# Kernel optimization log

Hardware: AMD Instinct MI355X
Metric: run time of the kernel (lower is better)

## Reference

```python
import jax, jax.numpy as jnp
import numpy as np

# Grid / module constants (init_kwargs)
SCALE_MULT = 3.0
H, W, D = 200, 200, 16
PC_MIN = np.array([-40.0, -40.0, -1.0], dtype=np.float32)
GRID = 0.4
RADII_MIN = 1
EPS = 1e-8

P, G, C = 16384, 2048, 17


def _quat_to_rot(q):
    # q: (..., 4) normalized quaternion -> (..., 3, 3)
    w, x, y, z = q[..., 0], q[..., 1], q[..., 2], q[..., 3]
    R = jnp.stack([
        1 - 2 * (y * y + z * z), 2 * (x * y - w * z), 2 * (x * z + w * y),
        2 * (x * y + w * z), 1 - 2 * (x * x + z * z), 2 * (y * z - w * x),
        2 * (x * z - w * y), 2 * (y * z + w * x), 1 - 2 * (x * x + y * y),
    ], axis=-1)
    return R.reshape(q.shape[:-1] + (3, 3))


def setup_inputs() -> dict:
    key = jax.random.key(0)
    ks = jax.random.split(key, 8)
    extent = jnp.asarray([H * GRID, W * GRID, D * GRID], jnp.float32)
    pc_min = jnp.asarray(PC_MIN)
    # points and primitive means strictly inside the grid (bounds asserts in the module)
    pts = pc_min + jax.random.uniform(ks[0], (1, P, 3), jnp.float32) * (extent - 1e-3)
    means3D = pc_min + jax.random.uniform(ks[1], (1, G, 3), jnp.float32) * (extent - 1e-3)
    opas = jax.random.uniform(ks[2], (1, G), jnp.float32, 0.05, 0.95)
    u = jax.random.uniform(ks[3], (1, G), jnp.float32, 0.5, 2.0)   # superquadric exponent e1
    v = jax.random.uniform(ks[4], (1, G), jnp.float32, 0.5, 2.0)   # superquadric exponent e2
    semantics = jax.random.normal(ks[5], (1, G, C), jnp.float32)
    scales = jax.random.uniform(ks[6], (1, G, 3), jnp.float32, 0.1, 0.6)
    q = jax.random.normal(ks[7], (1, G, 4), jnp.float32)
    q = q / jnp.linalg.norm(q, axis=-1, keepdims=True)
    rot3D = _quat_to_rot(q)  # (1, G, 3, 3)
    return {"pts": pts, "means3D": means3D, "opas": opas, "u": u, "v": v,
            "semantics": semantics, "scales": scales, "rot3D": rot3D}


def _forward(pts, means3D, opas, u, v, semantics, scales, rot3D):
    # squeeze batch dim of 1 (module asserts pts.shape[0] == 1)
    pts = pts[0]; means3D = means3D[0]; opas = opas[0]
    u = u[0]; v = v[0]; semantics = semantics[0]
    scales = scales[0]; rot3D = rot3D[0]
    pc_min = jnp.asarray(PC_MIN)

    points_int = jnp.floor((pts - pc_min) / GRID).astype(jnp.int32)              # (P,3)
    means_int = jnp.floor((jax.lax.stop_gradient(means3D) - pc_min) / GRID).astype(jnp.int32)  # (G,3)
    radii = jnp.ceil(jax.lax.stop_gradient(scales).max(-1) * SCALE_MULT / GRID).astype(jnp.int32)
    radii = jnp.maximum(radii, RADII_MIN)                                        # (G,)

    # radius-limited neighborhood (Chebyshev distance in voxel space)
    cheb = jnp.abs(points_int[:, None, :] - means_int[None, :, :]).max(-1)       # (P,G)
    mask = cheb <= radii[None, :]

    # local coords: R^T (p - mu), computed without materializing (P,G,3) deltas twice
    local = jnp.einsum('pj,gji->pgi', pts, rot3D) - jnp.einsum('gj,gji->gi', means3D, rot3D)[None]
    s2 = (local / scales[None]) ** 2 + EPS                                       # (P,G,3)

    inv_e1 = (1.0 / u)[None]  # (1,G)
    inv_e2 = (1.0 / v)[None]
    # superquadric inside-outside function
    f = (s2[..., 0] ** inv_e2 + s2[..., 1] ** inv_e2) ** (v / u)[None] + s2[..., 2] ** inv_e1
    a = opas[None] * jnp.exp(-0.5 * f)
    a = jnp.where(mask, a, 0.0)                                                  # (P,G)

    density = a.sum(-1)                                                          # (P,)
    logits = jnp.einsum('pg,gc->pc', a, semantics) / (density[:, None] + 1e-9)   # (P,C)
    a_c = jnp.clip(a, 0.0, 1.0 - 1e-4)
    bin_logits = 1.0 - jnp.exp(jnp.log1p(-a_c).sum(-1))                          # (P,)
    return logits, bin_logits, density


def reference(pts, means3D, opas, u, v, semantics, scales, rot3D):
    return _forward(pts, means3D, opas, u, v, semantics, scales, rot3D)
```

## Files before the change

### kernel.cpp

```cpp
#include <hip/hip_runtime.h>
#include <math.h>

#define NP 16384
#define NG 2048
#define NC 17

#define TSH 3
#define NTX 25
#define NTY 25
#define NTILE (NTX * NTY)
#define SEGC 32
#define CCAP 128
#define ROWF 40

#define GRIDSZ 0.4f
#define PCMINX -40.0f
#define PCMINY -40.0f
#define PCMINZ -1.0f
#define SCALE_MULTC 3.0f


__global__ __launch_bounds__(256)
void bin_kernel(const float* __restrict__ means3D, const float* __restrict__ opas,
                const float* __restrict__ uu, const float* __restrict__ vv,
                const float* __restrict__ semantics, const float* __restrict__ scales,
                const float* __restrict__ rot3D,
                unsigned int* __restrict__ candCnt, float* __restrict__ rowTbl) {
    __shared__ unsigned short candSeg[4][SEGC];
    __shared__ int wc[4];
    const int tid = threadIdx.x;
    const int lane = tid & 63;
    const int w = tid >> 6;
    const int b = blockIdx.x;
    const int tx = b % NTX, ty = b / NTX;

    unsigned cl = 0;
#pragma unroll
    for (int it = 0; it < 8; ++it) {
        int g = w * 512 + it * 64 + lane;
        float mx = means3D[g * 3 + 0], my = means3D[g * 3 + 1];
        float sx = scales[g * 3 + 0], sy = scales[g * 3 + 1], sz = scales[g * 3 + 2];
        int vx = (int)floorf((mx - PCMINX) / GRIDSZ);
        int vy = (int)floorf((my - PCMINY) / GRIDSZ);
        float smax = fmaxf(sx, fmaxf(sy, sz));
        int rad = (int)ceilf(smax * SCALE_MULTC / GRIDSZ);
        if (rad < 1) rad = 1;
        bool ov = (((vx - rad) >> TSH) <= tx) & (((vx + rad) >> TSH) >= tx) &
                  (((vy - rad) >> TSH) <= ty) & (((vy + rad) >> TSH) >= ty);
        unsigned long long bal = __ballot(ov);
        if (ov) {
            int pos = (int)cl + (int)__popcll(bal & ((1ull << lane) - 1ull));
            if (pos < SEGC) candSeg[w][pos] = (unsigned short)g;
        }
        cl += (unsigned)__popcll(bal);
    }
    if (lane == 0) wc[w] = min((int)cl, SEGC);
    __syncthreads();

    const int c0 = wc[0], c1 = wc[1], c2 = wc[2], c3 = wc[3];
    const int o1 = c0, o2 = o1 + c1, o3 = o2 + c2;
    const int total = o3 + c3;

    if (tid < total) {
        int s, idx;
        if (tid < o1)      { s = 0; idx = tid; }
        else if (tid < o2) { s = 1; idx = tid - o1; }
        else if (tid < o3) { s = 2; idx = tid - o2; }
        else               { s = 3; idx = tid - o3; }
        int g = (int)candSeg[s][idx];
        float mx = means3D[g * 3 + 0], my = means3D[g * 3 + 1], mz = means3D[g * 3 + 2];
        float sx = scales[g * 3 + 0], sy = scales[g * 3 + 1], sz = scales[g * 3 + 2];
        float r[9];
#pragma unroll
        for (int i = 0; i < 9; ++i) r[i] = rot3D[g * 9 + i];
        float sem[NC];
#pragma unroll
        for (int c = 0; c < NC; ++c) sem[c] = semantics[(size_t)g * NC + c];
        float ug = uu[g], vg = vv[g], op = opas[g];
        int vx = (int)floorf((mx - PCMINX) / GRIDSZ);
        int vy = (int)floorf((my - PCMINY) / GRIDSZ);
        int vz = (int)floorf((mz - PCMINZ) / GRIDSZ);
        float smax = fmaxf(sx, fmaxf(sy, sz));
        int rad = (int)ceilf(smax * SCALE_MULTC / GRIDSZ);
        if (rad < 1) rad = 1;

        float4* Rv = (float4*)(rowTbl + ((size_t)b * CCAP + tid) * ROWF);
        Rv[0] = make_float4(mx * r[0] + my * r[3] + mz * r[6],
                            mx * r[1] + my * r[4] + mz * r[7],
                            mx * r[2] + my * r[5] + mz * r[8], r[0]);
        Rv[1] = make_float4(r[1], r[2], r[3], r[4]);
        Rv[2] = make_float4(r[5], r[6], r[7], r[8]);
        Rv[3] = make_float4(1.0f / sx, 1.0f / sy, 1.0f / sz, op);
        Rv[4] = make_float4(1.0f / ug, 1.0f / vg, vg / ug, sem[16]);
        Rv[5] = make_float4(sem[0], sem[1], sem[2], sem[3]);
        Rv[6] = make_float4(sem[4], sem[5], sem[6], sem[7]);
        Rv[7] = make_float4(sem[8], sem[9], sem[10], sem[11]);
        Rv[8] = make_float4(sem[12], sem[13], sem[14], sem[15]);
        Rv[9] = make_float4(__int_as_float(vx), __int_as_float(vy),
                            __int_as_float(vz), __int_as_float(rad));
    }
    if (tid == 0) candCnt[b] = (unsigned)total;
}

__device__ __forceinline__ float eval_row(const float* __restrict__ R,
                                          float px, float py, float pz,
                                          int ix, int iy, int iz) {
    const float4* Rv = (const float4*)R;
    float4 f0 = Rv[0], f1 = Rv[1], f2 = Rv[2], f3 = Rv[3], f4 = Rv[4], f9 = Rv[9];
    int cheb = max(max(abs(ix - __float_as_int(f9.x)),
                       abs(iy - __float_as_int(f9.y))),
                   abs(iz - __float_as_int(f9.z)));
    float l0 = px * f0.w + py * f1.z + pz * f2.y - f0.x;
    float l1 = px * f1.x + py * f1.w + pz * f2.z - f0.y;
    float l2 = px * f1.y + py * f2.x + pz * f2.w - f0.z;
    float t0 = l0 * f3.x, t1 = l1 * f3.y, t2 = l2 * f3.z;
    float s0 = t0 * t0 + 1e-8f;
    float s1 = t1 * t1 + 1e-8f;
    float s2 = t2 * t2 + 1e-8f;
    float f = __powf(__powf(s0, f4.y) + __powf(s1, f4.y), f4.z) + __powf(s2, f4.x);
    float a = f3.w * __expf(-0.5f * f);
    return (cheb <= __float_as_int(f9.w)) ? a : 0.0f;
}

__global__ __launch_bounds__(256)
void point_kernel(const float* __restrict__ pts,
                  const unsigned int* __restrict__ candCnt,
                  const float* __restrict__ rowTbl,
                  float* __restrict__ out) {
    const int tid = threadIdx.x;
    const int lane = tid & 63;
    const int w = tid >> 6;
    const int sub = lane >> 4;
    const int k = lane & 15;
    const int p = blockIdx.x * 16 + w * 4 + sub;

    float px = pts[p * 3 + 0], py = pts[p * 3 + 1], pz = pts[p * 3 + 2];
    int ix = (int)floorf((px - PCMINX) / GRIDSZ);
    int iy = (int)floorf((py - PCMINY) / GRIDSZ);
    int iz = (int)floorf((pz - PCMINZ) / GRIDSZ);
    int t = (iy >> TSH) * NTX + (ix >> TSH);
    int n = (int)candCnt[t];
    const float* base = rowTbl + (size_t)t * CCAP * ROWF;

    float dens = 0.0f, lb = 0.0f, acc = 0.0f, acc16 = 0.0f;

    for (int j = 0; j * 16 < n; ++j) {
        int kk = j * 16 + k;
        float a = 0.0f;
        if (kk < n)
            a = eval_row(base + (size_t)kk * ROWF, px, py, pz, ix, iy, iz);
        dens += a;
        lb += __logf(1.0f - fminf(a, 1.0f - 1e-4f));

        int kmax = min(16, n - j * 16);
        for (int kq = 0; kq < kmax; ++kq) {
            float aq = __shfl(a, (sub << 4) + kq);
            const float* R = base + (size_t)(j * 16 + kq) * ROWF;
            acc = fmaf(aq, R[20 + k], acc);
            if (k == 0) acc16 = fmaf(aq, R[19], acc16);
        }
    }

#pragma unroll
    for (int o = 1; o < 16; o <<= 1) {
        dens += __shfl_xor(dens, o);
        lb += __shfl_xor(lb, o);
    }

    float inv = 1.0f / (dens + 1e-9f);
    out[(size_t)p * NC + k] = acc * inv;
    if (k == 0) {
        out[(size_t)p * NC + 16] = acc16 * inv;
        out[(size_t)NP * NC + p] = 1.0f - expf(lb);
        out[(size_t)NP * NC + NP + p] = dens;
    }
}

__global__ __launch_bounds__(64)
void agg_kernel_fb(const float* __restrict__ pts,
                   const float* __restrict__ means3D,
                   const float* __restrict__ opas,
                   const float* __restrict__ uu,
                   const float* __restrict__ vv,
                   const float* __restrict__ semantics,
                   const float* __restrict__ scales,
                   const float* __restrict__ rot3D,
                   float* __restrict__ out) {
    int p = blockIdx.x * 64 + threadIdx.x;
    if (p >= NP) return;
    float px = pts[p * 3 + 0], py = pts[p * 3 + 1], pz = pts[p * 3 + 2];
    int pix = (int)floorf((px - PCMINX) / GRIDSZ);
    int piy = (int)floorf((py - PCMINY) / GRIDSZ);
    int piz = (int)floorf((pz - PCMINZ) / GRIDSZ);
    float density = 0.0f, logbin = 0.0f;
    float acc[NC];
#pragma unroll
    for (int c = 0; c < NC; ++c) acc[c] = 0.0f;
    for (int g = 0; g < NG; ++g) {
        float mx = means3D[g * 3 + 0], my = means3D[g * 3 + 1], mz = means3D[g * 3 + 2];
        float sx = scales[g * 3 + 0], sy = scales[g * 3 + 1], sz = scales[g * 3 + 2];
        int vx = (int)floorf((mx - PCMINX) / GRIDSZ);
        int vy = (int)floorf((my - PCMINY) / GRIDSZ);
        int vz = (int)floorf((mz - PCMINZ) / GRIDSZ);
        float smax = fmaxf(sx, fmaxf(sy, sz));
        int rad = (int)ceilf(smax * SCALE_MULTC / GRIDSZ);
        rad = rad < 1 ? 1 : rad;
        int cheb = max(abs(pix - vx), max(abs(piy - vy), abs(piz - vz)));
        if (cheb <= rad) {
            const float* r = rot3D + (size_t)g * 9;
            float dx = px - mx, dy = py - my, dz = pz - mz;
            float l0 = dx * r[0] + dy * r[3] + dz * r[6];
            float l1 = dx * r[1] + dy * r[4] + dz * r[7];
            float l2 = dx * r[2] + dy * r[5] + dz * r[8];
            float t0 = l0 / sx, t1 = l1 / sy, t2 = l2 / sz;
            float s0 = t0 * t0 + 1e-8f, s1 = t1 * t1 + 1e-8f, s2 = t2 * t2 + 1e-8f;
            float ie1 = 1.0f / uu[g], ie2 = 1.0f / vv[g], e21 = vv[g] * ie1;
            float f = __powf(__powf(s0, ie2) + __powf(s1, ie2), e21) + __powf(s2, ie1);
            float a = opas[g] * __expf(-0.5f * f);
            density += a;
            const float* sg = semantics + (size_t)g * NC;
#pragma unroll
            for (int c = 0; c < NC; ++c) acc[c] = fmaf(a, sg[c], acc[c]);
            logbin += __logf(1.0f - fminf(a, 1.0f - 1e-4f));
        }
    }
    float inv = 1.0f / (density + 1e-9f);
#pragma unroll
    for (int c = 0; c < NC; ++c) out[(size_t)p * NC + c] = acc[c] * inv;
    out[(size_t)NP * NC + p] = 1.0f - expf(logbin);
    out[(size_t)NP * NC + NP + p] = density;
}

extern "C" void kernel_launch(void* const* d_in, const int* in_sizes, int n_in,
                              void* d_out, int out_size, void* d_ws, size_t ws_size,
                              hipStream_t stream) {
    const float* pts       = (const float*)d_in[0];
    const float* means3D   = (const float*)d_in[1];
    const float* opas      = (const float*)d_in[2];
    const float* uu        = (const float*)d_in[3];
    const float* vv        = (const float*)d_in[4];
    const float* semantics = (const float*)d_in[5];
    const float* scales    = (const float*)d_in[6];
    const float* rot3D     = (const float*)d_in[7];
    float* out = (float*)d_out;

    size_t cntBytes = ((size_t)NTILE * sizeof(unsigned int) + 255) & ~(size_t)255;
    size_t rowBytes = (size_t)NTILE * CCAP * ROWF * sizeof(float);
    size_t need = cntBytes + rowBytes;

    if (ws_size >= need) {
        unsigned int* candCnt = (unsigned int*)d_ws;
        float* rowTbl = (float*)((char*)d_ws + cntBytes);
        bin_kernel<<<NTILE, 256, 0, stream>>>(means3D, opas, uu, vv, semantics,
                                              scales, rot3D, candCnt, rowTbl);
        point_kernel<<<NP / 16, 256, 0, stream>>>(pts, candCnt, rowTbl, out);
    } else {
        agg_kernel_fb<<<NP / 64, 64, 0, stream>>>(pts, means3D, opas, uu, vv, semantics,
                                                  scales, rot3D, out);
    }
}
```

Baseline: 29.33 us.

## Pad candidate rows to multiples of 16, unroll accumulation, replace log-sum with product

The bin kernel zero-fills padding rows so each tile's candidate count is a multiple of 16. This lets the aggregation loop drop its bounds checks and fully unroll the 16-step shuffle/accumulate inner loop. The log1p/exp transmittance is replaced by a running product of (1-a) combined with multiplicative shuffles, which removes a log per element and the final exp. The ballot loop is also split from the overlap computation so the global loads can be batched. Zero rows give a=0 through opacity zero, but the product form may underflow differently than the log sum.

```diff
diff --git a/kernel.cpp b/kernel.cpp
--- a/kernel.cpp
+++ b/kernel.cpp
@@ -34,7 +34,7 @@
     const int b = blockIdx.x;
     const int tx = b % NTX, ty = b / NTX;
 
-    unsigned cl = 0;
+    bool ov[8];
 #pragma unroll
     for (int it = 0; it < 8; ++it) {
         int g = w * 512 + it * 64 + lane;
@@ -45,12 +45,16 @@
         float smax = fmaxf(sx, fmaxf(sy, sz));
         int rad = (int)ceilf(smax * SCALE_MULTC / GRIDSZ);
         if (rad < 1) rad = 1;
-        bool ov = (((vx - rad) >> TSH) <= tx) & (((vx + rad) >> TSH) >= tx) &
-                  (((vy - rad) >> TSH) <= ty) & (((vy + rad) >> TSH) >= ty);
-        unsigned long long bal = __ballot(ov);
-        if (ov) {
+        ov[it] = (((vx - rad) >> TSH) <= tx) & (((vx + rad) >> TSH) >= tx) &
+                 (((vy - rad) >> TSH) <= ty) & (((vy + rad) >> TSH) >= ty);
+    }
+    unsigned cl = 0;
+#pragma unroll
+    for (int it = 0; it < 8; ++it) {
+        unsigned long long bal = __ballot(ov[it]);
+        if (ov[it]) {
             int pos = (int)cl + (int)__popcll(bal & ((1ull << lane) - 1ull));
-            if (pos < SEGC) candSeg[w][pos] = (unsigned short)g;
+            if (pos < SEGC) candSeg[w][pos] = (unsigned short)(w * 512 + it * 64 + lane);
         }
         cl += (unsigned)__popcll(bal);
     }
@@ -60,6 +64,7 @@
     const int c0 = wc[0], c1 = wc[1], c2 = wc[2], c3 = wc[3];
     const int o1 = c0, o2 = o1 + c1, o3 = o2 + c2;
     const int total = o3 + c3;
+    const int pad = (total + 15) & ~15;
 
     if (tid < total) {
         int s, idx;
@@ -98,8 +103,13 @@
         Rv[8] = make_float4(sem[12], sem[13], sem[14], sem[15]);
         Rv[9] = make_float4(__int_as_float(vx), __int_as_float(vy),
                             __int_as_float(vz), __int_as_float(rad));
-    }
-    if (tid == 0) candCnt[b] = (unsigned)total;
+    } else if (tid < pad) {
+        float4* Rv = (float4*)(rowTbl + ((size_t)b * CCAP + tid) * ROWF);
+        float4 z = make_float4(0.0f, 0.0f, 0.0f, 0.0f);
+#pragma unroll
+        for (int i = 0; i < 10; ++i) Rv[i] = z;
+    }
+    if (tid == 0) candCnt[b] = (unsigned)pad;
 }
 
 __device__ __forceinline__ float eval_row(const float* __restrict__ R,
@@ -142,20 +152,17 @@
     int n = (int)candCnt[t];
     const float* base = rowTbl + (size_t)t * CCAP * ROWF;
 
-    float dens = 0.0f, lb = 0.0f, acc = 0.0f, acc16 = 0.0f;
-
-    for (int j = 0; j * 16 < n; ++j) {
-        int kk = j * 16 + k;
-        float a = 0.0f;
-        if (kk < n)
-            a = eval_row(base + (size_t)kk * ROWF, px, py, pz, ix, iy, iz);
+    float dens = 0.0f, prod = 1.0f, acc = 0.0f, acc16 = 0.0f;
+
+    for (int j = 0; j < n; j += 16) {
+        float a = eval_row(base + (size_t)(j + k) * ROWF, px, py, pz, ix, iy, iz);
         dens += a;
-        lb += __logf(1.0f - fminf(a, 1.0f - 1e-4f));
-
-        int kmax = min(16, n - j * 16);
-        for (int kq = 0; kq < kmax; ++kq) {
+        prod *= 1.0f - fminf(a, 1.0f - 1e-4f);
+
+#pragma unroll
+        for (int kq = 0; kq < 16; ++kq) {
             float aq = __shfl(a, (sub << 4) + kq);
-            const float* R = base + (size_t)(j * 16 + kq) * ROWF;
+            const float* R = base + (size_t)(j + kq) * ROWF;
             acc = fmaf(aq, R[20 + k], acc);
             if (k == 0) acc16 = fmaf(aq, R[19], acc16);
         }
@@ -164,14 +171,14 @@
 #pragma unroll
     for (int o = 1; o < 16; o <<= 1) {
         dens += __shfl_xor(dens, o);
-        lb += __shfl_xor(lb, o);
+        prod *= __shfl_xor(prod, o);
     }
 
     float inv = 1.0f / (dens + 1e-9f);
     out[(size_t)p * NC + k] = acc * inv;
     if (k == 0) {
         out[(size_t)p * NC + 16] = acc16 * inv;
-        out[(size_t)NP * NC + p] = 1.0f - expf(lb);
+        out[(size_t)NP * NC + p] = 1.0f - prod;
         out[(size_t)NP * NC + NP + p] = dens;
     }
 }
```

Measured after the change: 28.15 us. -4.0%, faster.
